# Optimization experiments

Hardware: AMD Instinct MI355X
Metric: run time of the kernel (lower is better)

Reference implementation:

```python
import jax, jax.numpy as jnp
import numpy as np

W_WIN = 4096   # number of octree windows
K = 32         # patch (window) size
C = 256        # dim
H = 8          # num_heads
D = C // H     # head dim
N = W_WIN * K  # total points
KC = 27        # 3x3x3 octree conv neighborhood
EPS = 1e-5


def layernorm(x, g, b):
    mu = jnp.mean(x, axis=-1, keepdims=True)
    var = jnp.var(x, axis=-1, keepdims=True)
    return (x - mu) * jax.lax.rsqrt(var + EPS) * g + b


def setup_inputs() -> dict:
    key = jax.random.key(0)
    ks = jax.random.split(key, 12)
    s = 0.02
    return {
        'data': jax.random.normal(ks[0], (N, C), jnp.float32),
        'relay_tokens': jax.random.normal(ks[1], (W_WIN, C), jnp.float32),
        'neigh': jax.random.randint(ks[2], (N, KC), 0, N, jnp.int32),
        # CPE: octree depthwise conv (27 taps) + batchnorm (eval, running stats)
        'cpe_w': jax.random.normal(ks[3], (KC, C), jnp.float32) * s,
        'bn_gamma': jnp.ones((C,), jnp.float32),
        'bn_beta': jnp.zeros((C,), jnp.float32),
        'bn_mean': jnp.zeros((C,), jnp.float32),
        'bn_var': jnp.ones((C,), jnp.float32),
        # norm1 / attention
        'norm1_g': jnp.ones((C,), jnp.float32),
        'norm1_b': jnp.zeros((C,), jnp.float32),
        'qkv_w': jax.random.normal(ks[4], (C, 3 * C), jnp.float32) * s,
        'qkv_b': jnp.zeros((3 * C,), jnp.float32),
        'proj_w': jax.random.normal(ks[5], (C, C), jnp.float32) * s,
        'proj_b': jnp.zeros((C,), jnp.float32),
        # norm2 / MLP
        'norm2_g': jnp.ones((C,), jnp.float32),
        'norm2_b': jnp.zeros((C,), jnp.float32),
        'fc1_w': jax.random.normal(ks[6], (C, 4 * C), jnp.float32) * s,
        'fc1_b': jnp.zeros((4 * C,), jnp.float32),
        'fc2_w': jax.random.normal(ks[7], (4 * C, C), jnp.float32) * s,
        'fc2_b': jnp.zeros((C,), jnp.float32),
    }


def _block(data, relay_tokens, neigh, cpe_w, bn_gamma, bn_beta, bn_mean, bn_var,
           norm1_g, norm1_b, qkv_w, qkv_b, proj_w, proj_b,
           norm2_g, norm2_b, fc1_w, fc1_b, fc2_w, fc2_b):
    # ---- CPE: depthwise octree conv + BN, residual ----
    acc = jnp.zeros_like(data)
    for k in range(KC):  # fixed small kernel loop; each gather is [N, C]
        acc = acc + data[neigh[:, k]] * cpe_w[k]
    cpe = (acc - bn_mean) * jax.lax.rsqrt(bn_var + EPS) * bn_gamma + bn_beta
    data = data + cpe

    # ---- data_to_windows + relay-token concat: [W, 1+K, C] ----
    x = data.reshape(W_WIN, K, C)
    x = jnp.concatenate([relay_tokens[:, None, :], x], axis=1)
    S = K + 1

    # ---- windowed MHA over each window (relay token + K points) ----
    h = layernorm(x, norm1_g, norm1_b)
    qkv = (h @ qkv_w + qkv_b).reshape(W_WIN, S, 3, H, D)
    q, kk, v = [jnp.moveaxis(qkv[:, :, i], 2, 1) for i in range(3)]  # [W,H,S,D]
    scale = D ** -0.5
    attn = jax.nn.softmax(jnp.einsum('whsd,whtd->whst', q * scale, kk), axis=-1)
    out = jnp.einsum('whst,whtd->whsd', attn, v)
    out = jnp.moveaxis(out, 1, 2).reshape(W_WIN, S, C)
    x = x + (out @ proj_w + proj_b)  # gamma1 = 1, drop_path = identity

    # ---- MLP residual ----
    h2 = layernorm(x, norm2_g, norm2_b)
    ffn = jax.nn.gelu(h2 @ fc1_w + fc1_b) @ fc2_w + fc2_b
    x = x + ffn  # gamma2 = 1

    # ---- split relay token / windows_to_data ----
    rt = x[:, 0, :]
    data_out = x[:, 1:, :].reshape(N, C)
    return data_out, rt


def reference(data, relay_tokens, neigh, cpe_w, bn_gamma, bn_beta, bn_mean, bn_var,
              norm1_g, norm1_b, qkv_w, qkv_b, proj_w, proj_b,
              norm2_g, norm2_b, fc1_w, fc1_b, fc2_w, fc2_b):
    return _block(data, relay_tokens, neigh, cpe_w, bn_gamma, bn_beta, bn_mean,
                  bn_var, norm1_g, norm1_b, qkv_w, qkv_b, proj_w, proj_b,
                  norm2_g, norm2_b, fc1_w, fc1_b, fc2_w, fc2_b)
```

## Files before the change

### kernel.cpp

```cpp
#include <hip/hip_runtime.h>

#define NW 4096
#define SEQ 33
#define CC 256
#define NTOK 131072
#define NKC 27

typedef unsigned short u16;
typedef __attribute__((ext_vector_type(8))) short s16x8;
typedef __attribute__((ext_vector_type(4))) short s16x4;
typedef __attribute__((ext_vector_type(4))) float f32x4;

#define MFMA16(a,b,c) __builtin_amdgcn_mfma_f32_16x16x32_bf16((a),(b),(c),0,0,0)

__device__ __forceinline__ float bu2f(u16 u){ return __uint_as_float(((unsigned int)u)<<16); }
__device__ __forceinline__ u16 f2bu(float f){
  unsigned int u = __float_as_uint(f);
  return (u16)((u + 0x7FFFu + ((u>>16)&1u)) >> 16);
}

__global__ void k_cvt(const float* __restrict__ in, u16* __restrict__ out, int n4){
  int stride = gridDim.x * blockDim.x;
  for (int i = blockIdx.x*blockDim.x + threadIdx.x; i < n4; i += stride){
    float4 v = ((const float4*)in)[i];
    s16x4 o;
    o[0] = (short)f2bu(v.x); o[1] = (short)f2bu(v.y);
    o[2] = (short)f2bu(v.z); o[3] = (short)f2bu(v.w);
    ((s16x4*)out)[i] = o;
  }
}

__global__ void k_tr(const float* __restrict__ in, u16* __restrict__ out, int R, int C){
  int stride = gridDim.x * blockDim.x;
  int total = R*C;
  for (int i = blockIdx.x*blockDim.x + threadIdx.x; i < total; i += stride){
    int r = i / C, c = i - r*C;
    out[c*R + r] = f2bu(in[i]);
  }
}

__global__ void k_relay(const float* __restrict__ rt, u16* __restrict__ xg){
  int stride = gridDim.x * blockDim.x;
  for (int i = blockIdx.x*blockDim.x + threadIdx.x; i < NW*CC; i += stride){
    int w = i >> 8, c = i & 255;
    xg[(w*SEQ)*CC + c] = f2bu(rt[i]);
  }
}

__global__ void k_cpe(const float* __restrict__ data, const u16* __restrict__ datab,
                      const int* __restrict__ neigh, const float* __restrict__ cpw,
                      const float* __restrict__ bng, const float* __restrict__ bnb,
                      const float* __restrict__ bnm, const float* __restrict__ bnv,
                      u16* __restrict__ xg){
  int n = blockIdx.x*8 + (threadIdx.x >> 5);
  int l = threadIdx.x & 31;
  int c0 = l*8;
  float a[8];
  #pragma unroll
  for (int j = 0; j < 8; ++j) a[j] = 0.f;
  const int* nr = neigh + n*NKC;
  for (int k = 0; k < NKC; ++k){
    int idx = nr[k];
    s16x8 d = *(const s16x8*)(datab + idx*CC + c0);
    float4 w0 = *(const float4*)(cpw + k*CC + c0);
    float4 w1 = *(const float4*)(cpw + k*CC + c0 + 4);
    a[0] += bu2f((u16)d[0])*w0.x; a[1] += bu2f((u16)d[1])*w0.y;
    a[2] += bu2f((u16)d[2])*w0.z; a[3] += bu2f((u16)d[3])*w0.w;
    a[4] += bu2f((u16)d[4])*w1.x; a[5] += bu2f((u16)d[5])*w1.y;
    a[6] += bu2f((u16)d[6])*w1.z; a[7] += bu2f((u16)d[7])*w1.w;
  }
  s16x8 o;
  #pragma unroll
  for (int half = 0; half < 2; ++half){
    float4 dv = *(const float4*)(data + n*CC + c0 + half*4);
    float4 g  = *(const float4*)(bng + c0 + half*4);
    float4 b  = *(const float4*)(bnb + c0 + half*4);
    float4 m  = *(const float4*)(bnm + c0 + half*4);
    float4 vv = *(const float4*)(bnv + c0 + half*4);
    float x0 = dv.x + (a[half*4+0] - m.x)*rsqrtf(vv.x + 1e-5f)*g.x + b.x;
    float x1 = dv.y + (a[half*4+1] - m.y)*rsqrtf(vv.y + 1e-5f)*g.y + b.y;
    float x2 = dv.z + (a[half*4+2] - m.z)*rsqrtf(vv.z + 1e-5f)*g.z + b.z;
    float x3 = dv.w + (a[half*4+3] - m.w)*rsqrtf(vv.w + 1e-5f)*g.w + b.w;
    o[half*4+0] = (short)f2bu(x0); o[half*4+1] = (short)f2bu(x1);
    o[half*4+2] = (short)f2bu(x2); o[half*4+3] = (short)f2bu(x3);
  }
  int w = n >> 5, s = (n & 31) + 1;
  *(s16x8*)(xg + (w*SEQ + s)*CC + c0) = o;
}

struct SharedW {
  u16 xs[33][264];
  union { u16 hs[48][264]; u16 P[8][33][72]; } A;
  union { u16 Q[48][264];  u16 och[48][264]; } B;
  union { u16 K[48][264];  u16 mch[48][264]; } C2;
  u16 VT[256][72];
};
static_assert(sizeof(SharedW) <= 160*1024, "LDS budget (1 block/CU)");

__global__ __attribute__((amdgpu_flat_work_group_size(1024,1024), amdgpu_waves_per_eu(4,4)))
void k_window(
    const u16* __restrict__ xg,
    const u16* __restrict__ qkvT, const u16* __restrict__ projT,
    const u16* __restrict__ fc1T, const u16* __restrict__ fc2T,
    const float* __restrict__ n1g, const float* __restrict__ n1b,
    const float* __restrict__ qkvb, const float* __restrict__ projb,
    const float* __restrict__ n2g, const float* __restrict__ n2b,
    const float* __restrict__ fc1b, const float* __restrict__ fc2b,
    float* __restrict__ out)
{
  __shared__ __align__(16) SharedW L;
  const int tid  = threadIdx.x;
  const int lane = tid & 63;
  const int wid  = tid >> 6;
  const int l15  = lane & 15;
  const int lg8  = (lane >> 4) * 8;
  const int lg4  = (lane >> 4) * 4;
  const int w    = blockIdx.x;
  const f32x4 fzero = {0.f,0.f,0.f,0.f};

  {
    f32x4* p = (f32x4*)((char*)&L + sizeof(L.xs));
    const int n16 = (int)((sizeof(SharedW) - sizeof(L.xs))/16);
    for (int i = tid; i < n16; i += 1024) p[i] = fzero;
  }
  for (int ci = tid; ci < SEQ*32; ci += 1024){
    int r = ci >> 5, cp = (ci & 31) << 3;
    *(s16x8*)&L.xs[r][cp] = *(const s16x8*)(xg + (w*SEQ + r)*CC + cp);
  }
  __syncthreads();

  auto LN = [&](const float* gg, const float* bb){
    for (int r = wid; r < SEQ; r += 16){
      int c0 = lane*4;
      s16x4 xv = *(const s16x4*)&L.xs[r][c0];
      float v0 = bu2f((u16)xv[0]), v1 = bu2f((u16)xv[1]);
      float v2 = bu2f((u16)xv[2]), v3 = bu2f((u16)xv[3]);
      float s  = v0+v1+v2+v3;
      float s2 = v0*v0+v1*v1+v2*v2+v3*v3;
      #pragma unroll
      for (int msk = 1; msk < 64; msk <<= 1){
        s  += __shfl_xor(s, msk);
        s2 += __shfl_xor(s2, msk);
      }
      float mu = s * (1.f/256.f);
      float var = s2 * (1.f/256.f) - mu*mu;
      float rs = rsqrtf(var + 1e-5f);
      float4 gv = *(const float4*)(gg + c0);
      float4 bv = *(const float4*)(bb + c0);
      s16x4 o;
      o[0] = (short)f2bu((v0-mu)*rs*gv.x + bv.x);
      o[1] = (short)f2bu((v1-mu)*rs*gv.y + bv.y);
      o[2] = (short)f2bu((v2-mu)*rs*gv.z + bv.z);
      o[3] = (short)f2bu((v3-mu)*rs*gv.w + bv.w);
      *(s16x4*)&L.A.hs[r][c0] = o;
    }
  };
  LN(n1g, n1b);
  __syncthreads();

  {
    #pragma unroll 1
    for (int i = 0; i < 3; ++i){
      int n = wid*3 + i;
      int sel = n >> 4;
      int cn  = (n & 15)*16 + l15;
      int ncol = n*16 + l15;
      const u16* wrow = qkvT + ncol*CC + lg8;
      float bias = qkvb[ncol];
      f32x4 acc[3] = {fzero, fzero, fzero};
      #pragma unroll 1
      for (int kc = 0; kc < 2; ++kc){
        s16x8 bf[4];
        #pragma unroll
        for (int kk = 0; kk < 4; ++kk) bf[kk] = *(const s16x8*)(wrow + (kc*4 + kk)*32);
        #pragma unroll
        for (int kk = 0; kk < 4; ++kk)
          #pragma unroll
          for (int m = 0; m < 3; ++m){
            s16x8 a = *(const s16x8*)&L.A.hs[m*16 + l15][(kc*4 + kk)*32 + lg8];
            acc[m] = MFMA16(a, bf[kk], acc[m]);
          }
      }
      #pragma unroll
      for (int m = 0; m < 3; ++m)
        #pragma unroll
        for (int jj = 0; jj < 4; ++jj){
          int row = m*16 + lg4 + jj;
          float val = acc[m][jj] + bias;
          if (sel == 0)      L.B.Q[row][cn]  = f2bu(val*0.17677669529663687f);
          else if (sel == 1) L.C2.K[row][cn] = f2bu(val);
          else               L.VT[cn][row]   = f2bu(val);
        }
    }
  }
  __syncthreads();

  {
    const int h = wid & 7;
    const int half = wid >> 3;
    s16x8 bk[3];
    #pragma unroll
    for (int n = 0; n < 3; ++n) bk[n] = *(const s16x8*)&L.C2.K[n*16 + l15][h*32 + lg8];
    const int nm = half ? 1 : 2;
    for (int mi = 0; mi < nm; ++mi){
      int m = half ? 1 : (mi ? 2 : 0);
      s16x8 aq = *(const s16x8*)&L.B.Q[m*16 + l15][h*32 + lg8];
      f32x4 sc0 = MFMA16(aq, bk[0], fzero);
      f32x4 sc1 = MFMA16(aq, bk[1], fzero);
      f32x4 sc2 = MFMA16(aq, bk[2], fzero);
      #pragma unroll
      for (int jj = 0; jj < 4; ++jj){
        float a0 = sc0[jj];
        float a1 = sc1[jj];
        float a2 = (l15 == 0) ? sc2[jj] : -1e30f;
        float mx = fmaxf(fmaxf(a0, a1), a2);
        #pragma unroll
        for (int msk = 1; msk < 16; msk <<= 1) mx = fmaxf(mx, __shfl_xor(mx, msk));
        float e0 = __expf(a0 - mx), e1 = __expf(a1 - mx), e2 = __expf(a2 - mx);
        float sm = e0 + e1 + e2;
        #pragma unroll
        for (int msk = 1; msk < 16; msk <<= 1) sm += __shfl_xor(sm, msk);
        float inv = 1.f / sm;
        int row = m*16 + lg4 + jj;
        if (row < SEQ){
          L.A.P[h][row][l15]      = f2bu(e0*inv);
          L.A.P[h][row][16 + l15] = f2bu(e1*inv);
          L.A.P[h][row][32 + l15] = f2bu(e2*inv);
        }
      }
    }
  }
  __syncthreads();

  {
    const int h = wid & 7;
    const int half = wid >> 3;
    s16x8 bv0 = *(const s16x8*)&L.VT[h*32 + half*16 + l15][lg8];
    s16x8 bv1 = *(const s16x8*)&L.VT[h*32 + half*16 + l15][32 + lg8];
    int col = h*32 + half*16 + l15;
    #pragma unroll
    for (int m = 0; m < 3; ++m){
      int row = m*16 + l15; if (row > 32) row = 32;
      s16x8 pa0 = *(const s16x8*)&L.A.P[h][row][lg8];
      s16x8 pa1 = *(const s16x8*)&L.A.P[h][row][32 + lg8];
      f32x4 acc = MFMA16(pa0, bv0, fzero);
      acc = MFMA16(pa1, bv1, acc);
      #pragma unroll
      for (int jj = 0; jj < 4; ++jj)
        L.B.och[m*16 + lg4 + jj][col] = f2bu(acc[jj]);
    }
  }
  __syncthreads();

  {
    int ncol = wid*16 + l15;
    const u16* wrow = projT + ncol*CC + lg8;
    f32x4 acc[3] = {fzero, fzero, fzero};
    #pragma unroll 1
    for (int kc = 0; kc < 2; ++kc){
      s16x8 bf[4];
      #pragma unroll
      for (int kk = 0; kk < 4; ++kk) bf[kk] = *(const s16x8*)(wrow + (kc*4 + kk)*32);
      #pragma unroll
      for (int kk = 0; kk < 4; ++kk)
        #pragma unroll
        for (int m = 0; m < 3; ++m){
          s16x8 a = *(const s16x8*)&L.B.och[m*16 + l15][(kc*4 + kk)*32 + lg8];
          acc[m] = MFMA16(a, bf[kk], acc[m]);
        }
    }
    float pb = projb[ncol];
    #pragma unroll
    for (int m = 0; m < 3; ++m)
      #pragma unroll
      for (int jj = 0; jj < 4; ++jj){
        int row = m*16 + lg4 + jj;
        if (row < SEQ){
          float x = bu2f(L.xs[row][ncol]) + acc[m][jj] + pb;
          L.xs[row][ncol] = f2bu(x);
        }
      }
  }
  __syncthreads();

  LN(n2g, n2b);
  __syncthreads();

  f32x4 accF[3] = {fzero, fzero, fzero};

  #pragma unroll 1
  for (int nc = 0; nc < 4; ++nc){
    {
      int nl = wid*16 + l15;
      int ncol = nc*256 + nl;
      const u16* wrow = fc1T + ncol*CC + lg8;
      float bias = fc1b[ncol];
      f32x4 acc[3] = {fzero, fzero, fzero};
      #pragma unroll 1
      for (int kc = 0; kc < 2; ++kc){
        s16x8 bf[4];
        #pragma unroll
        for (int kk = 0; kk < 4; ++kk) bf[kk] = *(const s16x8*)(wrow + (kc*4 + kk)*32);
        #pragma unroll
        for (int kk = 0; kk < 4; ++kk)
          #pragma unroll
          for (int m = 0; m < 3; ++m){
            s16x8 a = *(const s16x8*)&L.A.hs[m*16 + l15][(kc*4 + kk)*32 + lg8];
            acc[m] = MFMA16(a, bf[kk], acc[m]);
          }
      }
      #pragma unroll
      for (int m = 0; m < 3; ++m)
        #pragma unroll
        for (int jj = 0; jj < 4; ++jj){
          int row = m*16 + lg4 + jj;
          float xv = acc[m][jj] + bias;
          float z2 = 1.5957691216057308f*(xv + 0.044715f*xv*xv*xv);
          float gl = xv / (1.f + __expf(-z2));
          L.C2.mch[row][nl] = f2bu(gl);
        }
    }
    __syncthreads();
    {
      const u16* wrow = fc2T + (wid*16 + l15)*1024 + nc*256 + lg8;
      #pragma unroll 1
      for (int kc = 0; kc < 2; ++kc){
        s16x8 bf[4];
        #pragma unroll
        for (int kk = 0; kk < 4; ++kk) bf[kk] = *(const s16x8*)(wrow + (kc*4 + kk)*32);
        #pragma unroll
        for (int kk = 0; kk < 4; ++kk)
          #pragma unroll
          for (int m = 0; m < 3; ++m){
            s16x8 a = *(const s16x8*)&L.C2.mch[m*16 + l15][(kc*4 + kk)*32 + lg8];
            accF[m] = MFMA16(a, bf[kk], accF[m]);
          }
      }
    }
    __syncthreads();
  }

  {
    int col = wid*16 + l15;
    float fb = fc2b[col];
    #pragma unroll
    for (int m = 0; m < 3; ++m)
      #pragma unroll
      for (int jj = 0; jj < 4; ++jj){
        int row = m*16 + lg4 + jj;
        if (row < SEQ){
          float x = bu2f(L.xs[row][col]) + accF[m][jj] + fb;
          if (row == 0) out[NTOK*CC + w*CC + col] = x;
          else          out[(w*32 + row - 1)*CC + col] = x;
        }
      }
  }
}

extern "C" void kernel_launch(void* const* d_in, const int* in_sizes, int n_in,
                              void* d_out, int out_size, void* d_ws, size_t ws_size,
                              hipStream_t stream){
  const float* data  = (const float*)d_in[0];
  const float* relay = (const float*)d_in[1];
  const int*   neigh = (const int*)d_in[2];
  const float* cpw   = (const float*)d_in[3];
  const float* bng   = (const float*)d_in[4];
  const float* bnb   = (const float*)d_in[5];
  const float* bnm   = (const float*)d_in[6];
  const float* bnv   = (const float*)d_in[7];
  const float* n1g   = (const float*)d_in[8];
  const float* n1b   = (const float*)d_in[9];
  const float* qkvw  = (const float*)d_in[10];
  const float* qkvb  = (const float*)d_in[11];
  const float* projw = (const float*)d_in[12];
  const float* projb = (const float*)d_in[13];
  const float* n2g   = (const float*)d_in[14];
  const float* n2b   = (const float*)d_in[15];
  const float* fc1w  = (const float*)d_in[16];
  const float* fc1b  = (const float*)d_in[17];
  const float* fc2w  = (const float*)d_in[18];
  const float* fc2b  = (const float*)d_in[19];

  char* ws = (char*)d_ws;
  u16* datab = (u16*)ws;
  u16* xg    = (u16*)(ws + 67108864);
  u16* qkvT  = (u16*)(ws + 136314880);
  u16* projT = (u16*)(ws + 136708096);
  u16* fc1T  = (u16*)(ws + 136839168);
  u16* fc2T  = (u16*)(ws + 137363456);

  k_cvt<<<4096, 256, 0, stream>>>(data, datab, NTOK*CC/4);
  k_tr<<<256, 256, 0, stream>>>(qkvw, qkvT, 256, 768);
  k_tr<<<256, 256, 0, stream>>>(projw, projT, 256, 256);
  k_tr<<<256, 256, 0, stream>>>(fc1w, fc1T, 256, 1024);
  k_tr<<<256, 256, 0, stream>>>(fc2w, fc2T, 1024, 256);
  k_relay<<<1024, 256, 0, stream>>>(relay, xg);
  k_cpe<<<NTOK/8, 256, 0, stream>>>(data, datab, neigh, cpw, bng, bnb, bnm, bnv, xg);
  k_window<<<NW, 1024, 0, stream>>>(xg, qkvT, projT, fc1T, fc2T,
                                    n1g, n1b, qkvb, projb, n2g, n2b, fc1b, fc2b,
                                    (float*)d_out);
}
```

Before: 1.475 ms.

## Double-buffer MLP hidden chunks and trim padded rows in window kernel

Shrinks the padded 48-row shared buffers to 33 rows. The third M-tile now reads only the real row 32 and stores are guarded to rows below SEQ. The P·V stage is merged into the softmax block, removing one barrier. The fc1/fc2 loop is software-pipelined with two ping-pong hidden buffers, so fc2 of chunk n and fc1 of chunk n+1 run between a single barrier instead of two. This is meant to cut barrier stalls and let MFMA work overlap, at the cost of more complex LDS aliasing: the och and K buffers are reused for the MLP chunks.

```diff
diff --git a/kernel.cpp b/kernel.cpp
--- a/kernel.cpp
+++ b/kernel.cpp
@@ -90,9 +90,10 @@
 
 struct SharedW {
   u16 xs[33][264];
-  union { u16 hs[48][264]; u16 P[8][33][72]; } A;
-  union { u16 Q[48][264];  u16 och[48][264]; } B;
-  union { u16 K[48][264];  u16 mch[48][264]; } C2;
+  union { u16 hs[33][264]; u16 P[8][33][72]; } A;
+  u16 Q[33][264];
+  union { u16 K[33][264];   u16 mch0[33][264]; } C2;
+  union { u16 och[33][264]; u16 mch1[33][264]; } D;
   u16 VT[256][72];
 };
 static_assert(sizeof(SharedW) <= 160*1024, "LDS budget (1 block/CU)");
@@ -177,7 +178,8 @@
         for (int kk = 0; kk < 4; ++kk)
           #pragma unroll
           for (int m = 0; m < 3; ++m){
-            s16x8 a = *(const s16x8*)&L.A.hs[m*16 + l15][(kc*4 + kk)*32 + lg8];
+            int ar = (m == 2) ? 32 : (m*16 + l15);
+            s16x8 a = *(const s16x8*)&L.A.hs[ar][(kc*4 + kk)*32 + lg8];
             acc[m] = MFMA16(a, bf[kk], acc[m]);
           }
       }
@@ -186,10 +188,12 @@
         #pragma unroll
         for (int jj = 0; jj < 4; ++jj){
           int row = m*16 + lg4 + jj;
-          float val = acc[m][jj] + bias;
-          if (sel == 0)      L.B.Q[row][cn]  = f2bu(val*0.17677669529663687f);
-          else if (sel == 1) L.C2.K[row][cn] = f2bu(val);
-          else               L.VT[cn][row]   = f2bu(val);
+          if (row < SEQ){
+            float val = acc[m][jj] + bias;
+            if (sel == 0)      L.Q[row][cn]    = f2bu(val*0.17677669529663687f);
+            else if (sel == 1) L.C2.K[row][cn] = f2bu(val);
+            else               L.VT[cn][row]   = f2bu(val);
+          }
         }
     }
   }
@@ -198,16 +202,17 @@
   {
     const int h = wid & 7;
     const int half = wid >> 3;
-    s16x8 bk[3];
-    #pragma unroll
-    for (int n = 0; n < 3; ++n) bk[n] = *(const s16x8*)&L.C2.K[n*16 + l15][h*32 + lg8];
+    s16x8 bk0 = *(const s16x8*)&L.C2.K[l15][h*32 + lg8];
+    s16x8 bk1 = *(const s16x8*)&L.C2.K[16 + l15][h*32 + lg8];
+    s16x8 bk2 = *(const s16x8*)&L.C2.K[32][h*32 + lg8];
     const int nm = half ? 1 : 2;
     for (int mi = 0; mi < nm; ++mi){
       int m = half ? 1 : (mi ? 2 : 0);
-      s16x8 aq = *(const s16x8*)&L.B.Q[m*16 + l15][h*32 + lg8];
-      f32x4 sc0 = MFMA16(aq, bk[0], fzero);
-      f32x4 sc1 = MFMA16(aq, bk[1], fzero);
-      f32x4 sc2 = MFMA16(aq, bk[2], fzero);
+      int ar = (m == 2) ? 32 : (m*16 + l15);
+      s16x8 aq = *(const s16x8*)&L.Q[ar][h*32 + lg8];
+      f32x4 sc0 = MFMA16(aq, bk0, fzero);
+      f32x4 sc1 = MFMA16(aq, bk1, fzero);
+      f32x4 sc2 = MFMA16(aq, bk2, fzero);
       #pragma unroll
       for (int jj = 0; jj < 4; ++jj){
         float a0 = sc0[jj];
@@ -229,25 +234,28 @@
         }
       }
     }
-  }
-  __syncthreads();
-
-  {
-    const int h = wid & 7;
-    const int half = wid >> 3;
-    s16x8 bv0 = *(const s16x8*)&L.VT[h*32 + half*16 + l15][lg8];
-    s16x8 bv1 = *(const s16x8*)&L.VT[h*32 + half*16 + l15][32 + lg8];
-    int col = h*32 + half*16 + l15;
+    s16x8 bva[2], bvb[2];
     #pragma unroll
-    for (int m = 0; m < 3; ++m){
-      int row = m*16 + l15; if (row > 32) row = 32;
-      s16x8 pa0 = *(const s16x8*)&L.A.P[h][row][lg8];
-      s16x8 pa1 = *(const s16x8*)&L.A.P[h][row][32 + lg8];
-      f32x4 acc = MFMA16(pa0, bv0, fzero);
-      acc = MFMA16(pa1, bv1, acc);
-      #pragma unroll
-      for (int jj = 0; jj < 4; ++jj)
-        L.B.och[m*16 + lg4 + jj][col] = f2bu(acc[jj]);
+    for (int nd = 0; nd < 2; ++nd){
+      bva[nd] = *(const s16x8*)&L.VT[h*32 + nd*16 + l15][lg8];
+      bvb[nd] = *(const s16x8*)&L.VT[h*32 + nd*16 + l15][32 + lg8];
+    }
+    for (int mi = 0; mi < nm; ++mi){
+      int m = half ? 1 : (mi ? 2 : 0);
+      int pr = (m == 2) ? 32 : (m*16 + l15);
+      s16x8 pa0 = *(const s16x8*)&L.A.P[h][pr][lg8];
+      s16x8 pa1 = *(const s16x8*)&L.A.P[h][pr][32 + lg8];
+      #pragma unroll
+      for (int nd = 0; nd < 2; ++nd){
+        f32x4 acc = MFMA16(pa0, bva[nd], fzero);
+        acc = MFMA16(pa1, bvb[nd], acc);
+        #pragma unroll
+        for (int jj = 0; jj < 4; ++jj){
+          int row = m*16 + lg4 + jj;
+          if (row < SEQ)
+            L.D.och[row][h*32 + nd*16 + l15] = f2bu(acc[jj]);
+        }
+      }
     }
   }
   __syncthreads();
@@ -265,7 +273,8 @@
       for (int kk = 0; kk < 4; ++kk)
         #pragma unroll
         for (int m = 0; m < 3; ++m){
-          s16x8 a = *(const s16x8*)&L.B.och[m*16 + l15][(kc*4 + kk)*32 + lg8];
+          int ar = (m == 2) ? 32 : (m*16 + l15);
+          s16x8 a = *(const s16x8*)&L.D.och[ar][(kc*4 + kk)*32 + lg8];
           acc[m] = MFMA16(a, bf[kk], acc[m]);
         }
     }
@@ -288,57 +297,66 @@
 
   f32x4 accF[3] = {fzero, fzero, fzero};
 
-  #pragma unroll 1
-  for (int nc = 0; nc < 4; ++nc){
-    {
-      int nl = wid*16 + l15;
-      int ncol = nc*256 + nl;
-      const u16* wrow = fc1T + ncol*CC + lg8;
-      float bias = fc1b[ncol];
-      f32x4 acc[3] = {fzero, fzero, fzero};
-      #pragma unroll 1
-      for (int kc = 0; kc < 2; ++kc){
-        s16x8 bf[4];
-        #pragma unroll
-        for (int kk = 0; kk < 4; ++kk) bf[kk] = *(const s16x8*)(wrow + (kc*4 + kk)*32);
-        #pragma unroll
-        for (int kk = 0; kk < 4; ++kk)
-          #pragma unroll
-          for (int m = 0; m < 3; ++m){
-            s16x8 a = *(const s16x8*)&L.A.hs[m*16 + l15][(kc*4 + kk)*32 + lg8];
-            acc[m] = MFMA16(a, bf[kk], acc[m]);
-          }
-      }
-      #pragma unroll
-      for (int m = 0; m < 3; ++m)
-        #pragma unroll
-        for (int jj = 0; jj < 4; ++jj){
-          int row = m*16 + lg4 + jj;
+  auto FC1 = [&](int nc, u16 (*mch)[264]){
+    int nl = wid*16 + l15;
+    int ncol = nc*256 + nl;
+    const u16* wrow = fc1T + ncol*CC + lg8;
+    float bias = fc1b[ncol];
+    f32x4 acc[3] = {fzero, fzero, fzero};
+    #pragma unroll 1
+    for (int kc = 0; kc < 2; ++kc){
+      s16x8 bf[4];
+      #pragma unroll
+      for (int kk = 0; kk < 4; ++kk) bf[kk] = *(const s16x8*)(wrow + (kc*4 + kk)*32);
+      #pragma unroll
+      for (int kk = 0; kk < 4; ++kk)
+        #pragma unroll
+        for (int m = 0; m < 3; ++m){
+          int ar = (m == 2) ? 32 : (m*16 + l15);
+          s16x8 a = *(const s16x8*)&L.A.hs[ar][(kc*4 + kk)*32 + lg8];
+          acc[m] = MFMA16(a, bf[kk], acc[m]);
+        }
+    }
+    #pragma unroll
+    for (int m = 0; m < 3; ++m)
+      #pragma unroll
+      for (int jj = 0; jj < 4; ++jj){
+        int row = m*16 + lg4 + jj;
+        if (row < SEQ){
           float xv = acc[m][jj] + bias;
           float z2 = 1.5957691216057308f*(xv + 0.044715f*xv*xv*xv);
           float gl = xv / (1.f + __expf(-z2));
-          L.C2.mch[row][nl] = f2bu(gl);
-        }
-    }
-    __syncthreads();
-    {
-      const u16* wrow = fc2T + (wid*16 + l15)*1024 + nc*256 + lg8;
-      #pragma unroll 1
-      for (int kc = 0; kc < 2; ++kc){
-        s16x8 bf[4];
-        #pragma unroll
-        for (int kk = 0; kk < 4; ++kk) bf[kk] = *(const s16x8*)(wrow + (kc*4 + kk)*32);
-        #pragma unroll
-        for (int kk = 0; kk < 4; ++kk)
-          #pragma unroll
-          for (int m = 0; m < 3; ++m){
-            s16x8 a = *(const s16x8*)&L.C2.mch[m*16 + l15][(kc*4 + kk)*32 + lg8];
-            accF[m] = MFMA16(a, bf[kk], accF[m]);
-          }
-      }
-    }
-    __syncthreads();
-  }
+          mch[row][nl] = f2bu(gl);
+        }
+      }
+  };
+  auto FC2 = [&](int nc, const u16 (*mch)[264]){
+    const u16* wrow = fc2T + (wid*16 + l15)*1024 + nc*256 + lg8;
+    #pragma unroll 1
+    for (int kc = 0; kc < 2; ++kc){
+      s16x8 bf[4];
+      #pragma unroll
+      for (int kk = 0; kk < 4; ++kk) bf[kk] = *(const s16x8*)(wrow + (kc*4 + kk)*32);
+      #pragma unroll
+      for (int kk = 0; kk < 4; ++kk)
+        #pragma unroll
+        for (int m = 0; m < 3; ++m){
+          int ar = (m == 2) ? 32 : (m*16 + l15);
+          s16x8 a = *(const s16x8*)&mch[ar][(kc*4 + kk)*32 + lg8];
+          accF[m] = MFMA16(a, bf[kk], accF[m]);
+        }
+    }
+  };
+
+  FC1(0, L.C2.mch0);
+  __syncthreads();
+  FC2(0, L.C2.mch0); FC1(1, L.D.mch1);
+  __syncthreads();
+  FC2(1, L.D.mch1);  FC1(2, L.C2.mch0);
+  __syncthreads();
+  FC2(2, L.C2.mch0); FC1(3, L.D.mch1);
+  __syncthreads();
+  FC2(3, L.D.mch1);
 
   {
     int col = wid*16 + l15;
```

After: 1.435 ms. -2.7%, faster.
